# Kernel tuning notes

Measured on AMD Instinct MI355X. Metric: run time of the kernel, lower is better.

Reference implementation:

```python
import jax, jax.numpy as jnp
from jax import lax
import numpy as np

# Model dims (see shape_source)
D_MODEL = 768
N_LAYERS = 8
D_STATE = 16
EXPAND = 2
D_INNER = EXPAND * D_MODEL          # 1536
DT_RANK = (D_MODEL + 15) // 16       # 48
D_CONV = 4
PATCH = 16
IMG = 224
CH = 3
BATCH = 8


def rmsnorm(x, w, eps=1e-5):
    return x * lax.rsqrt(jnp.mean(x * x, axis=-1, keepdims=True) + eps) * w


def patch_embed(img, w, b):
    # img: [B,C,H,W] -> tokens [B, N, d_model]
    x = lax.conv_general_dilated(img, w, (PATCH, PATCH), 'VALID',
                                 dimension_numbers=('NCHW', 'OIHW', 'NCHW'))
    x = x + b[None, :, None, None]
    Bsz = img.shape[0]
    return x.reshape(Bsz, D_MODEL, -1).transpose(0, 2, 1)


def mamba_block(x, in_w, cw, cb, xw, dtw, dtb, a_log, d_p, ow):
    # x: [B, L, d_model]
    Bsz, L, _ = x.shape
    xz = x @ in_w.T                                   # [B,L,2*ED]
    xin, z = jnp.split(xz, 2, axis=-1)
    # causal depthwise conv over L
    xc = lax.conv_general_dilated(xin.transpose(0, 2, 1), cw, (1,),
                                  [(D_CONV - 1, 0)],
                                  dimension_numbers=('NCH', 'OIH', 'NCH'),
                                  feature_group_count=D_INNER)
    xin = jax.nn.silu((xc + cb[None, :, None]).transpose(0, 2, 1))  # [B,L,ED]
    dbc = xin @ xw.T                                  # [B,L,dt_rank+2N]
    delta, Bm, Cm = jnp.split(dbc, [DT_RANK, DT_RANK + D_STATE], axis=-1)
    delta = jax.nn.softplus(delta @ dtw.T + dtb)      # [B,L,ED]
    A = -jnp.exp(a_log)                               # [ED,N]
    dA = jnp.exp(delta[..., None] * A)                # [B,L,ED,N]
    dBx = (delta * xin)[..., None] * Bm[:, :, None, :]  # [B,L,ED,N]

    def step(h, inp):
        a, bx = inp
        h = a * h + bx
        return h, h

    h0 = jnp.zeros((Bsz, D_INNER, D_STATE), x.dtype)
    _, hs = lax.scan(step, h0, (dA.transpose(1, 0, 2, 3), dBx.transpose(1, 0, 2, 3)))
    y = jnp.einsum('lben,bln->ble', hs, Cm)           # [B,L,ED]
    y = y + d_p * xin
    y = y * jax.nn.silu(z)
    return y @ ow.T                                   # [B,L,d_model]


def setup_inputs() -> dict:
    key = jax.random.key(0)
    ks = jax.random.split(key, 16)
    s = 0.02
    nl = N_LAYERS
    inp = {
        'rgb': jax.random.normal(ks[0], (BATCH, CH, IMG, IMG), jnp.float32),
        't': jax.random.normal(ks[1], (BATCH, CH, IMG, IMG), jnp.float32),
        'pe_w': jax.random.normal(ks[2], (D_MODEL, CH, PATCH, PATCH), jnp.float32) * s,
        'pe_b': jnp.zeros((D_MODEL,), jnp.float32),
        'in_proj_w': jax.random.normal(ks[3], (nl, 2 * D_INNER, D_MODEL), jnp.float32) * s,
        'conv_w': jax.random.normal(ks[4], (nl, D_INNER, 1, D_CONV), jnp.float32) * s,
        'conv_b': jnp.zeros((nl, D_INNER), jnp.float32),
        'x_proj_w': jax.random.normal(ks[5], (nl, DT_RANK + 2 * D_STATE, D_INNER), jnp.float32) * s,
        'dt_proj_w': jax.random.normal(ks[6], (nl, D_INNER, DT_RANK), jnp.float32) * s,
        'dt_proj_b': jax.random.normal(ks[7], (nl, D_INNER), jnp.float32) * s,
        'A_log': jnp.log(jnp.broadcast_to(jnp.arange(1.0, D_STATE + 1.0), (nl, D_INNER, D_STATE))),
        'D': jnp.ones((nl, D_INNER), jnp.float32),
        'out_proj_w': jax.random.normal(ks[8], (nl, D_MODEL, D_INNER), jnp.float32) * s,
        'norm_w': jnp.ones((nl, D_MODEL), jnp.float32),
    }
    return inp


def reference(rgb, t, pe_w, pe_b, in_proj_w, conv_w, conv_b, x_proj_w,
              dt_proj_w, dt_proj_b, A_log, D, out_proj_w, norm_w):
    rt = patch_embed(rgb, pe_w, pe_b)   # [B,196,768]
    tt = patch_embed(t, pe_w, pe_b)
    x = jnp.concatenate([rt, tt], axis=1)  # [B,392,768]
    for i in range(N_LAYERS):
        x = x + mamba_block(rmsnorm(x, norm_w[i]), in_proj_w[i], conv_w[i],
                            conv_b[i], x_proj_w[i], dt_proj_w[i], dt_proj_b[i],
                            A_log[i], D[i], out_proj_w[i])
    Bsz = rgb.shape[0]
    # [B,2N,D] -> [B,2N,D,1] -> transpose(0,3) -> [1,2N,D,B] -> [2B,C,H,W]
    out = jnp.transpose(x[..., None], (3, 1, 2, 0)).reshape(2 * Bsz, CH, IMG, IMG)
    return out[:Bsz], out[Bsz:]
```

## Files before the change

kernel.cpp:

```cpp
#include <hip/hip_runtime.h>
#include <cstddef>
#include <cstdint>

#define L_TOK 392
#define BATCH 8
#define DM    768
#define ED    1536
#define NST   16
#define DTR   48
#define ROWS  (BATCH * L_TOK)

#define C_CH 8
#define CLEN 49
#define EGB  24

#define XP_Z  6


typedef unsigned short ushortT;
typedef __bf16 bf16x8 __attribute__((ext_vector_type(8)));
typedef unsigned short us8 __attribute__((ext_vector_type(8)));
typedef unsigned short us4 __attribute__((ext_vector_type(4)));
typedef float f32x4 __attribute__((ext_vector_type(4)));

#define LOG2E 1.4426950408889634f

__device__ __forceinline__ float bf2f(ushortT u) {
    union { unsigned int i; float f; } v; v.i = ((unsigned int)u) << 16; return v.f;
}
__device__ __forceinline__ ushortT f2bf(float f) {
    union { float f; unsigned int i; } v; v.f = f;
    unsigned int r = v.i + 0x7FFFu + ((v.i >> 16) & 1u);
    return (ushortT)(r >> 16);
}

__device__ __forceinline__ void gload16(const void* g, void* l) {
    __builtin_amdgcn_global_load_lds(
        (const __attribute__((address_space(1))) void*)g,
        (__attribute__((address_space(3))) void*)l, 16, 0, 0);
}

enum { EPI_STORE = 0, EPI_BIAS = 1, EPI_BIAS_SOFTPLUS = 2, EPI_ADD = 3 };

__global__ __launch_bounds__(256)
void convert3_kernel(const float* __restrict__ s0, ushortT* __restrict__ d0, int n0,
                     const float* __restrict__ s1, ushortT* __restrict__ d1, int n1,
                     const float* __restrict__ s2, ushortT* __restrict__ d2, int n2)
{
    int idx = blockIdx.x * 256 + threadIdx.x;
    const float* s; ushortT* d;
    if (idx < n0) { s = s0; d = d0; }
    else if (idx < n0 + n1) { idx -= n0; s = s1; d = d1; }
    else if (idx < n0 + n1 + n2) { idx -= n0 + n1; s = s2; d = d2; }
    else return;
    float4 f = *(const float4*)(s + (size_t)idx * 4);
    us4 h; h.x = f2bf(f.x); h.y = f2bf(f.y); h.z = f2bf(f.z); h.w = f2bf(f.w);
    *(us4*)(d + (size_t)idx * 4) = h;
}

template <int EPI, bool C_BF, bool SPLIT, bool ATOMIC, bool PARTIAL>
__global__ __launch_bounds__(256)
void gemm_mfma(const ushortT* __restrict__ A, int lda,
               const ushortT* __restrict__ W, int ldw,
               const float* __restrict__ bias,
               void* __restrict__ Cv, void* __restrict__ Cv2, int ldc,
               int M, int N, int K, int kchunk)
{
    __shared__ ushortT As[2][128 * 32];
    __shared__ ushortT Ws[2][128 * 32];

    const int tid  = threadIdx.x;
    const int lane = tid & 63;
    const int wave = tid >> 6;
    const int wm   = wave >> 1;
    const int wn   = wave & 1;
    const int quad = lane >> 4;
    const int l16  = lane & 15;

    const int gx   = gridDim.x;
    const int nwg  = gx * gridDim.y;
    const int flat = blockIdx.y * gx + blockIdx.x;
    const int q = nwg >> 3, r = nwg & 7;
    const int xcd = flat & 7, sidx = flat >> 3;
    const int swz = (xcd < r ? xcd * (q + 1) : r * (q + 1) + (xcd - r) * q) + sidx;

    const int m0 = (swz / gx) * 128;
    const int n0 = (swz % gx) * 128;
    const int kb = blockIdx.z * kchunk;
    const int KT = kchunk / 32;

    const int srow = lane >> 2;
    const int scol = (lane & 3) * 8;
    const ushortT* aBase = A + (size_t)(m0 + srow) * lda + scol;
    const ushortT* wBase = W + (size_t)(n0 + srow) * ldw + scol;

    auto stage = [&](int buf, int k0) {
#pragma unroll
        for (int c = 0; c < 2; ++c) {
            const int seg = wave * 2 + c;
            gload16(aBase + (size_t)(seg * 16) * lda + k0, &As[buf][seg * 512]);
            gload16(wBase + (size_t)(seg * 16) * ldw + k0, &Ws[buf][seg * 512]);
        }
    };

    f32x4 acc[4][4] = {};

    auto compute = [&](int buf) {
        bf16x8 af[4], bw[4];
#pragma unroll
        for (int t = 0; t < 4; ++t) {
            us8 ta = *(const us8*)&As[buf][(wm * 64 + t * 16 + l16) * 32 + quad * 8];
            af[t] = __builtin_bit_cast(bf16x8, ta);
            us8 tb = *(const us8*)&Ws[buf][(wn * 64 + t * 16 + l16) * 32 + quad * 8];
            bw[t] = __builtin_bit_cast(bf16x8, tb);
        }
#pragma unroll
        for (int i = 0; i < 4; ++i)
#pragma unroll
            for (int j = 0; j < 4; ++j)
                acc[i][j] = __builtin_amdgcn_mfma_f32_16x16x32_bf16(
                    af[i], bw[j], acc[i][j], 0, 0, 0);
    };

    stage(0, kb);
    __syncthreads();

    for (int kt = 0; kt < KT; ++kt) {
        if (kt + 1 < KT) stage((kt & 1) ^ 1, kb + (kt + 1) * 32);
        compute(kt & 1);
        __syncthreads();
    }

#pragma unroll
    for (int i = 0; i < 4; ++i) {
#pragma unroll
        for (int r2 = 0; r2 < 4; ++r2) {
            int gm = m0 + wm * 64 + i * 16 + quad * 4 + r2;
            if (gm >= M) continue;
#pragma unroll
            for (int j = 0; j < 4; ++j) {
                int gn = n0 + wn * 64 + j * 16 + l16;
                if (gn >= N) continue;
                float v = acc[i][j][r2];
                if (EPI == EPI_BIAS) v += bias[gn];
                void* dst = Cv;
                int cn = gn;
                if (SPLIT && gn >= ED) { dst = Cv2; cn = gn - ED; }
                size_t off = (size_t)gm * ldc + cn;
                if (PARTIAL) {
                    ((float*)dst)[(size_t)blockIdx.z * M * ldc + off] = v;
                } else if (ATOMIC) {
                    atomicAdd((float*)dst + off, v);
                } else if (C_BF) {
                    ((ushortT*)dst)[off] = f2bf(v);
                } else {
                    float* p = (float*)dst + off;
                    *p = (EPI == EPI_ADD) ? v + *p : v;
                }
            }
        }
    }
}

__global__ __launch_bounds__(256)
void reduce_partials_kernel(const float* __restrict__ P, float* __restrict__ dbc)
{
    int idx = blockIdx.x * 256 + threadIdx.x;
    if (idx >= ROWS * 80) return;
    float s = 0.f;
#pragma unroll
    for (int z = 0; z < XP_Z; ++z)
        s += P[(size_t)z * ROWS * 80 + idx];
    dbc[idx] = s;
}

template <int EPI, bool A_BF, bool C_BF>
__global__ __launch_bounds__(256)
void gemm_nt(const void* __restrict__ Av, int lda,
             const float* __restrict__ W, int ldw,
             const float* __restrict__ bias,
             void* __restrict__ Cv, int ldc,
             int M, int N, int K)
{
    __shared__ float As[16][68];
    __shared__ float Bs[16][68];
    const int tid = threadIdx.x;
    const int tx  = tid & 15;
    const int ty  = tid >> 4;
    const int bm  = blockIdx.y * 64;
    const int bn  = blockIdx.x * 64;
    const int lr  = tid >> 2;
    const int lk  = (tid & 3) * 4;

    float acc[4][4] = {};

    for (int k0 = 0; k0 < K; k0 += 16) {
        float a0 = 0.f, a1 = 0.f, a2 = 0.f, a3 = 0.f;
        float w0 = 0.f, w1 = 0.f, w2 = 0.f, w3 = 0.f;
        int ga = bm + lr;
        if (ga < M) {
            if (A_BF) {
                const ushortT* A = (const ushortT*)Av;
                ushort4 t = *(const ushort4*)(A + (size_t)ga * lda + k0 + lk);
                a0 = bf2f(t.x); a1 = bf2f(t.y); a2 = bf2f(t.z); a3 = bf2f(t.w);
            } else {
                const float* A = (const float*)Av;
                float4 t = *(const float4*)(A + (size_t)ga * lda + k0 + lk);
                a0 = t.x; a1 = t.y; a2 = t.z; a3 = t.w;
            }
        }
        int gw = bn + lr;
        if (gw < N) {
            float4 t = *(const float4*)(W + (size_t)gw * ldw + k0 + lk);
            w0 = t.x; w1 = t.y; w2 = t.z; w3 = t.w;
        }
        As[lk + 0][lr] = a0; As[lk + 1][lr] = a1;
        As[lk + 2][lr] = a2; As[lk + 3][lr] = a3;
        Bs[lk + 0][lr] = w0; Bs[lk + 1][lr] = w1;
        Bs[lk + 2][lr] = w2; Bs[lk + 3][lr] = w3;
        __syncthreads();
#pragma unroll
        for (int k = 0; k < 16; ++k) {
            float4 a4 = *(const float4*)&As[k][ty * 4];
            float4 b4 = *(const float4*)&Bs[k][tx * 4];
            float a[4] = {a4.x, a4.y, a4.z, a4.w};
            float b[4] = {b4.x, b4.y, b4.z, b4.w};
#pragma unroll
            for (int i = 0; i < 4; ++i)
#pragma unroll
                for (int j = 0; j < 4; ++j)
                    acc[i][j] += a[i] * b[j];
        }
        __syncthreads();
    }

#pragma unroll
    for (int i = 0; i < 4; ++i) {
        int gm = bm + ty * 4 + i;
        if (gm >= M) continue;
#pragma unroll
        for (int j = 0; j < 4; ++j) {
            int gn = bn + tx * 4 + j;
            if (gn >= N) continue;
            float v = acc[i][j];
            if (EPI == EPI_BIAS) v += bias[gn];
            if (EPI == EPI_BIAS_SOFTPLUS) {
                v += bias[gn];
                v = fmaxf(v, 0.f) + log1pf(expf(-fabsf(v)));
            }
            size_t off = (size_t)gm * ldc + gn;
            if (C_BF) {
                ((ushortT*)Cv)[off] = f2bf(v);
            } else {
                float* p = (float*)Cv + off;
                *p = (EPI == EPI_ADD) ? v + *p : v;
            }
        }
    }
}

__global__ __launch_bounds__(256)
void rmsnorm_kernel(const float* __restrict__ x, const float* __restrict__ w,
                    ushortT* __restrict__ xn)
{
    int r = blockIdx.x;
    const float* xr = x + (size_t)r * DM;
    float v[3];
    float s = 0.f;
#pragma unroll
    for (int i = 0; i < 3; ++i) {
        v[i] = xr[threadIdx.x + i * 256];
        s += v[i] * v[i];
    }
#pragma unroll
    for (int o = 32; o > 0; o >>= 1) s += __shfl_down(s, o, 64);
    __shared__ float wsum[4];
    __shared__ float scale_s;
    int wave = threadIdx.x >> 6;
    if ((threadIdx.x & 63) == 0) wsum[wave] = s;
    __syncthreads();
    if (threadIdx.x == 0) {
        float t = wsum[0] + wsum[1] + wsum[2] + wsum[3];
        scale_s = rsqrtf(t * (1.f / 768.f) + 1e-5f);
    }
    __syncthreads();
    float sc = scale_s;
#pragma unroll
    for (int i = 0; i < 3; ++i) {
        int d = threadIdx.x + i * 256;
        xn[(size_t)r * DM + d] = f2bf(v[i] * sc * w[d]);
    }
}

__global__ __launch_bounds__(256)
void conv_silu_kernel(const ushortT* __restrict__ xc, const float* __restrict__ cw,
                      const float* __restrict__ cb, ushortT* __restrict__ xin)
{
    int idx = blockIdx.x * 256 + threadIdx.x;
    if (idx >= ROWS * ED) return;
    int e = idx % ED;
    int r = idx / ED;
    int l = r % L_TOK;
    float w0 = cw[e * 4 + 0], w1 = cw[e * 4 + 1];
    float w2 = cw[e * 4 + 2], w3 = cw[e * 4 + 3];
    const ushortT* base = xc + (size_t)r * ED + e;
    float acc = cb[e] + w3 * bf2f(base[0]);
    if (l >= 1) acc += w2 * bf2f(base[-(ptrdiff_t)ED]);
    if (l >= 2) acc += w1 * bf2f(base[-(ptrdiff_t)(2 * ED)]);
    if (l >= 3) acc += w0 * bf2f(base[-(ptrdiff_t)(3 * ED)]);
    xin[(size_t)r * ED + e] = f2bf(acc / (1.f + __expf(-acc)));
}

__global__ __launch_bounds__(64)
void scan_part1(const ushortT* __restrict__ delta, const ushortT* __restrict__ xin,
                const float* __restrict__ dbc, const float* __restrict__ a_log,
                float* __restrict__ hend, float* __restrict__ sdl)
{
    __shared__ float BsL[CLEN * 16];
    const int tid = threadIdx.x;
    const int bid = blockIdx.x;
    const int eg = bid % EGB;
    const int c  = (bid / EGB) % C_CH;
    const int b  = bid / (EGB * C_CH);
    const int e  = eg * 64 + tid;
    const int l0 = c * CLEN;
    const int rb = b * L_TOK + l0;

    for (int i = tid; i < CLEN * 16; i += 64) {
        int s = i >> 4, n = i & 15;
        BsL[i] = dbc[(size_t)(rb + s) * 80 + 48 + n];
    }
    __syncthreads();

    float a[16];
    const float* ar = a_log + (size_t)e * 16;
#pragma unroll
    for (int n = 0; n < 16; ++n) a[n] = -__expf(ar[n]) * LOG2E;

    float h[16];
#pragma unroll
    for (int n = 0; n < 16; ++n) h[n] = 0.f;
    float sum_dl = 0.f;

    const size_t base = (size_t)rb * ED + e;
    float rdl[7], rxi[7];
#pragma unroll
    for (int j = 0; j < 7; ++j) {
        rdl[j] = bf2f(delta[base + (size_t)j * ED]);
        rxi[j] = bf2f(xin[base + (size_t)j * ED]);
    }
    for (int s0 = 0; s0 < CLEN; s0 += 7) {
#pragma unroll
        for (int j = 0; j < 7; ++j) {
            const int s = s0 + j;
            float dl = rdl[j], xi = rxi[j];
            int sp = s + 7; if (sp > CLEN - 1) sp = CLEN - 1;
            rdl[j] = bf2f(delta[base + (size_t)sp * ED]);
            rxi[j] = bf2f(xin[base + (size_t)sp * ED]);
            float dlxi = dl * xi;
            sum_dl += dl;
#pragma unroll
            for (int n = 0; n < 16; ++n)
                h[n] = __builtin_amdgcn_exp2f(dl * a[n]) * h[n] + dlxi * BsL[s * 16 + n];
        }
    }

    float* hp = hend + (((size_t)b * ED + e) * C_CH + c) * 16;
#pragma unroll
    for (int n = 0; n < 16; ++n) hp[n] = h[n];
    sdl[((size_t)b * ED + e) * C_CH + c] = sum_dl;
}

__global__ __launch_bounds__(64)
void scan_part2(const ushortT* __restrict__ delta, const ushortT* __restrict__ xin,
                const float* __restrict__ dbc, const ushortT* __restrict__ zb,
                const float* __restrict__ a_log, const float* __restrict__ dvec,
                const float* __restrict__ hend, const float* __restrict__ sdl,
                ushortT* __restrict__ y)
{
    __shared__ float BsL[CLEN * 16];
    __shared__ float CsL[CLEN * 16];
    const int tid = threadIdx.x;
    const int bid = blockIdx.x;
    const int eg = bid % EGB;
    const int c  = (bid / EGB) % C_CH;
    const int b  = bid / (EGB * C_CH);
    const int e  = eg * 64 + tid;
    const int l0 = c * CLEN;
    const int rb = b * L_TOK + l0;

    for (int i = tid; i < CLEN * 16; i += 64) {
        int s = i >> 4, n = i & 15;
        size_t row = (size_t)(rb + s) * 80;
        BsL[i] = dbc[row + 48 + n];
        CsL[i] = dbc[row + 64 + n];
    }
    __syncthreads();

    float a[16];
    const float* ar = a_log + (size_t)e * 16;
#pragma unroll
    for (int n = 0; n < 16; ++n) a[n] = -__expf(ar[n]) * LOG2E;
    const float dcf = dvec[e];

    float h[16];
#pragma unroll
    for (int n = 0; n < 16; ++n) h[n] = 0.f;
    const float* hb = hend + (((size_t)b * ED + e) * C_CH) * 16;
    const float* sb = sdl + ((size_t)b * ED + e) * C_CH;
    for (int cc = 0; cc < c; ++cc) {
        float sv = sb[cc];
#pragma unroll
        for (int n = 0; n < 16; ++n)
            h[n] = __builtin_amdgcn_exp2f(a[n] * sv) * h[n] + hb[cc * 16 + n];
    }

    const size_t base = (size_t)rb * ED + e;
    float rdl[7], rxi[7], rz[7];
#pragma unroll
    for (int j = 0; j < 7; ++j) {
        rdl[j] = bf2f(delta[base + (size_t)j * ED]);
        rxi[j] = bf2f(xin[base + (size_t)j * ED]);
        rz[j]  = bf2f(zb[base + (size_t)j * ED]);
    }
    for (int s0 = 0; s0 < CLEN; s0 += 7) {
#pragma unroll
        for (int j = 0; j < 7; ++j) {
            const int s = s0 + j;
            float dl = rdl[j], xi = rxi[j], z = rz[j];
            int sp = s + 7; if (sp > CLEN - 1) sp = CLEN - 1;
            rdl[j] = bf2f(delta[base + (size_t)sp * ED]);
            rxi[j] = bf2f(xin[base + (size_t)sp * ED]);
            rz[j]  = bf2f(zb[base + (size_t)sp * ED]);
            float dlxi = dl * xi;
            float yv = 0.f;
#pragma unroll
            for (int n = 0; n < 16; ++n) {
                h[n] = __builtin_amdgcn_exp2f(dl * a[n]) * h[n] + dlxi * BsL[s * 16 + n];
                yv += h[n] * CsL[s * 16 + n];
            }
            yv += dcf * xi;
            float sz = z / (1.f + __expf(-z));
            y[base + (size_t)s * ED] = f2bf(yv * sz);
        }
    }
}

__global__ __launch_bounds__(256)
void im2col_kernel(const float* __restrict__ rgb, const float* __restrict__ timg,
                   ushortT* __restrict__ P)
{
    int idx = blockIdx.x * 256 + threadIdx.x;
    if (idx >= ROWS * DM) return;
    int k = idx % DM;
    int r = idx / DM;
    int b = r / L_TOK;
    int l = r % L_TOK;
    const float* img = (l < 196) ? rgb : timg;
    int p  = (l < 196) ? l : l - 196;
    int py = p / 14, px = p % 14;
    int c  = k >> 8;
    int ph = (k >> 4) & 15;
    int pw = k & 15;
    P[idx] = f2bf(img[(((size_t)b * 3 + c) * 224 + (py * 16 + ph)) * 224 + (px * 16 + pw)]);
}

__global__ __launch_bounds__(256)
void out_transpose_kernel(const float* __restrict__ x, float* __restrict__ out)
{
    int idx = blockIdx.x * 256 + threadIdx.x;
    if (idx >= ROWS * DM) return;
    int b = idx & 7;
    int d = (idx >> 3) % DM;
    int l = idx / (8 * DM);
    out[idx] = x[((size_t)(b * L_TOK + l)) * DM + d];
}

extern "C" void kernel_launch(void* const* d_in, const int* in_sizes, int n_in,
                              void* d_out, int out_size, void* d_ws, size_t ws_size,
                              hipStream_t stream)
{
    (void)in_sizes; (void)n_in; (void)out_size; (void)ws_size;

    const float* rgb  = (const float*)d_in[0];
    const float* timg = (const float*)d_in[1];
    const float* pe_w = (const float*)d_in[2];
    const float* pe_b = (const float*)d_in[3];
    const float* in_w = (const float*)d_in[4];
    const float* cw   = (const float*)d_in[5];
    const float* cb   = (const float*)d_in[6];
    const float* xw   = (const float*)d_in[7];
    const float* dtw  = (const float*)d_in[8];
    const float* dtb  = (const float*)d_in[9];
    const float* alog = (const float*)d_in[10];
    const float* dvec = (const float*)d_in[11];
    const float* ow   = (const float*)d_in[12];
    const float* nw   = (const float*)d_in[13];

    char* p = (char*)d_ws;
    float*   X   = (float*)p;    p += (size_t)ROWS * DM * 4;
    ushortT* XC  = (ushortT*)p;  p += (size_t)ROWS * ED * 2;
    ushortT* Zb  = (ushortT*)p;  p += (size_t)ROWS * ED * 2;
    ushortT* XIN = (ushortT*)p;  p += (size_t)ROWS * ED * 2;
    ushortT* DEL = (ushortT*)p;  p += (size_t)ROWS * ED * 2;
    float*   DBC = (float*)p;    p += (size_t)ROWS * 80 * 4;
    ushortT* XN  = DEL;

    ushortT* INWB = XIN;
    ushortT* XWB  = (ushortT*)DBC;
    ushortT* PEB  = Zb;

    float* POUT = (float*)d_out;
    float* HEND = (float*)d_out;
    float* SDL  = HEND + (size_t)BATCH * ED * C_CH * 16;
    ushortT* OWB = (ushortT*)((char*)d_out +
                   ((size_t)BATCH * ED * C_CH * 16 + (size_t)BATCH * ED * C_CH) * 4);

    dim3 b256(256);
    const int MT = (ROWS + 127) / 128;
    const int SCAN_BLOCKS = BATCH * C_CH * EGB;

    const int PE_F4  = DM * DM / 4;
    const int INW_F4 = 2 * ED * DM / 4;
    const int XW_F4  = 80 * ED / 4;
    const int OW_F4  = DM * ED / 4;
    const int CVT_BLOCKS = (INW_F4 + XW_F4 + OW_F4 + 255) / 256;

    convert3_kernel<<<(PE_F4 + 255) / 256, b256, 0, stream>>>(
        pe_w, PEB, PE_F4, nullptr, nullptr, 0, nullptr, nullptr, 0);
    im2col_kernel<<<(ROWS * DM + 255) / 256, b256, 0, stream>>>(rgb, timg, XC);
    gemm_mfma<EPI_BIAS, false, false, false, false><<<dim3(DM / 128, MT), b256, 0, stream>>>(
        XC, DM, PEB, DM, pe_b, X, nullptr, DM, ROWS, DM, DM, DM);

    for (int i = 0; i < 8; ++i) {
        const float* in_wi = in_w + (size_t)i * 2 * ED * DM;
        const float* cwi   = cw   + (size_t)i * ED * 4;
        const float* cbi   = cb   + (size_t)i * ED;
        const float* xwi   = xw   + (size_t)i * 80 * ED;
        const float* dtwi  = dtw  + (size_t)i * ED * DTR;
        const float* dtbi  = dtb  + (size_t)i * ED;
        const float* ali   = alog + (size_t)i * ED * NST;
        const float* dvi   = dvec + (size_t)i * ED;
        const float* owi   = ow   + (size_t)i * DM * ED;
        const float* nwi   = nw   + (size_t)i * DM;

        convert3_kernel<<<CVT_BLOCKS, b256, 0, stream>>>(
            in_wi, INWB, INW_F4, xwi, XWB, XW_F4, owi, OWB, OW_F4);
        rmsnorm_kernel<<<ROWS, b256, 0, stream>>>(X, nwi, XN);
        gemm_mfma<EPI_STORE, true, true, false, false><<<dim3(2 * ED / 128, MT), b256, 0, stream>>>(
            XN, DM, INWB, DM, nullptr, XC, Zb, ED, ROWS, 2 * ED, DM, DM);
        conv_silu_kernel<<<(ROWS * ED + 255) / 256, b256, 0, stream>>>(
            XC, cwi, cbi, XIN);
        gemm_mfma<EPI_STORE, false, false, false, true><<<dim3(1, MT, XP_Z), b256, 0, stream>>>(
            XIN, ED, XWB, ED, nullptr, POUT, nullptr, 80, ROWS, 80, ED, ED / XP_Z);
        reduce_partials_kernel<<<(ROWS * 80 + 255) / 256, b256, 0, stream>>>(
            POUT, DBC);
        gemm_nt<EPI_BIAS_SOFTPLUS, false, true><<<dim3(ED / 64, ROWS / 64), b256, 0, stream>>>(
            DBC, 80, dtwi, DTR, dtbi, DEL, ED, ROWS, ED, DTR);
        scan_part1<<<SCAN_BLOCKS, 64, 0, stream>>>(
            DEL, XIN, DBC, ali, HEND, SDL);
        scan_part2<<<SCAN_BLOCKS, 64, 0, stream>>>(
            DEL, XIN, DBC, Zb, ali, dvi, HEND, SDL, XC);
        gemm_mfma<EPI_ADD, false, false, true, false><<<dim3(DM / 128, MT, 2), b256, 0, stream>>>(
            XC, ED, OWB, ED, nullptr, X, nullptr, DM, ROWS, DM, ED, ED / 2);
    }

    out_transpose_kernel<<<(ROWS * DM + 255) / 256, b256, 0, stream>>>(
        X, (float*)d_out);
}
```

Before: 1.733 ms.

## Move dt_proj GEMM to bf16 MFMA and fuse rmsnorm with weight conversion

Replaces the scalar fp32 gemm_nt used for dt_proj (K=48) with the MFMA bf16 GEMM. The reduce kernel now also writes a bf16 copy of the delta rank slice padded to 64 columns, and the dt_proj weights are converted to a zero-padded bf16 layout. Softplus is added to the MFMA epilogue. Rmsnorm and the per-layer weight conversion are merged into one prep kernel to cut a launch per layer. The cost is a bf16 rounding of the delta inputs and weights, plus extra buffers placed in the output scratch space.

Result: slower. 1.793 ms (+3.4%).

```diff
diff --git a/kernel.cpp b/kernel.cpp
--- a/kernel.cpp
+++ b/kernel.cpp
@@ -58,6 +58,71 @@
     *(us4*)(d + (size_t)idx * 4) = h;
 }
 
+#define INW_F4 (2 * ED * DM / 4)
+#define XW_F4  (80 * ED / 4)
+#define OW_F4  (DM * ED / 4)
+#define DTW_U  (ED * 16)
+
+__global__ __launch_bounds__(256)
+void prep_kernel(const float* __restrict__ in_w, ushortT* __restrict__ inwb,
+                 const float* __restrict__ xw,   ushortT* __restrict__ xwb,
+                 const float* __restrict__ ow,   ushortT* __restrict__ owb,
+                 const float* __restrict__ dtw,  ushortT* __restrict__ dtwb,
+                 const float* __restrict__ x,    const float* __restrict__ nw,
+                 ushortT* __restrict__ xn)
+{
+    if (blockIdx.x < ROWS) {
+        int r = blockIdx.x;
+        const float* xr = x + (size_t)r * DM;
+        float v[3];
+        float s = 0.f;
+#pragma unroll
+        for (int i = 0; i < 3; ++i) {
+            v[i] = xr[threadIdx.x + i * 256];
+            s += v[i] * v[i];
+        }
+#pragma unroll
+        for (int o = 32; o > 0; o >>= 1) s += __shfl_down(s, o, 64);
+        __shared__ float wsum[4];
+        __shared__ float scale_s;
+        int wave = threadIdx.x >> 6;
+        if ((threadIdx.x & 63) == 0) wsum[wave] = s;
+        __syncthreads();
+        if (threadIdx.x == 0) {
+            float t = wsum[0] + wsum[1] + wsum[2] + wsum[3];
+            scale_s = rsqrtf(t * (1.f / 768.f) + 1e-5f);
+        }
+        __syncthreads();
+        float sc = scale_s;
+#pragma unroll
+        for (int i = 0; i < 3; ++i) {
+            int d = threadIdx.x + i * 256;
+            xn[(size_t)r * DM + d] = f2bf(v[i] * sc * nw[d]);
+        }
+        return;
+    }
+    int idx = (blockIdx.x - ROWS) * 256 + threadIdx.x;
+    if (idx < INW_F4 + XW_F4 + OW_F4) {
+        const float* s; ushortT* d;
+        if (idx < INW_F4) { s = in_w; d = inwb; }
+        else if (idx < INW_F4 + XW_F4) { idx -= INW_F4; s = xw; d = xwb; }
+        else { idx -= INW_F4 + XW_F4; s = ow; d = owb; }
+        float4 f = *(const float4*)(s + (size_t)idx * 4);
+        us4 h; h.x = f2bf(f.x); h.y = f2bf(f.y); h.z = f2bf(f.z); h.w = f2bf(f.w);
+        *(us4*)(d + (size_t)idx * 4) = h;
+    } else if (idx < INW_F4 + XW_F4 + OW_F4 + DTW_U) {
+        int u = idx - (INW_F4 + XW_F4 + OW_F4);
+        int row = u >> 4;
+        int c4  = (u & 15) * 4;
+        us4 h = {0, 0, 0, 0};
+        if (c4 < DTR) {
+            float4 f = *(const float4*)(dtw + (size_t)row * DTR + c4);
+            h.x = f2bf(f.x); h.y = f2bf(f.y); h.z = f2bf(f.z); h.w = f2bf(f.w);
+        }
+        *(us4*)(dtwb + (size_t)row * 64 + c4) = h;
+    }
+}
+
 template <int EPI, bool C_BF, bool SPLIT, bool ATOMIC, bool PARTIAL>
 __global__ __launch_bounds__(256)
 void gemm_mfma(const ushortT* __restrict__ A, int lda,
@@ -143,6 +208,10 @@
                 if (gn >= N) continue;
                 float v = acc[i][j][r2];
                 if (EPI == EPI_BIAS) v += bias[gn];
+                if (EPI == EPI_BIAS_SOFTPLUS) {
+                    v += bias[gn];
+                    v = fmaxf(v, 0.f) + log1pf(expf(-fabsf(v)));
+                }
                 void* dst = Cv;
                 int cn = gn;
                 if (SPLIT && gn >= ED) { dst = Cv2; cn = gn - ED; }
@@ -163,132 +232,24 @@
 }
 
 __global__ __launch_bounds__(256)
-void reduce_partials_kernel(const float* __restrict__ P, float* __restrict__ dbc)
+void reduce_partials_kernel(const float* __restrict__ P, float* __restrict__ dbc,
+                            ushortT* __restrict__ dbc48)
 {
     int idx = blockIdx.x * 256 + threadIdx.x;
-    if (idx >= ROWS * 80) return;
-    float s = 0.f;
-#pragma unroll
-    for (int z = 0; z < XP_Z; ++z)
-        s += P[(size_t)z * ROWS * 80 + idx];
-    dbc[idx] = s;
-}
-
-template <int EPI, bool A_BF, bool C_BF>
-__global__ __launch_bounds__(256)
-void gemm_nt(const void* __restrict__ Av, int lda,
-             const float* __restrict__ W, int ldw,
-             const float* __restrict__ bias,
-             void* __restrict__ Cv, int ldc,
-             int M, int N, int K)
-{
-    __shared__ float As[16][68];
-    __shared__ float Bs[16][68];
-    const int tid = threadIdx.x;
-    const int tx  = tid & 15;
-    const int ty  = tid >> 4;
-    const int bm  = blockIdx.y * 64;
-    const int bn  = blockIdx.x * 64;
-    const int lr  = tid >> 2;
-    const int lk  = (tid & 3) * 4;
-
-    float acc[4][4] = {};
-
-    for (int k0 = 0; k0 < K; k0 += 16) {
-        float a0 = 0.f, a1 = 0.f, a2 = 0.f, a3 = 0.f;
-        float w0 = 0.f, w1 = 0.f, w2 = 0.f, w3 = 0.f;
-        int ga = bm + lr;
-        if (ga < M) {
-            if (A_BF) {
-                const ushortT* A = (const ushortT*)Av;
-                ushort4 t = *(const ushort4*)(A + (size_t)ga * lda + k0 + lk);
-                a0 = bf2f(t.x); a1 = bf2f(t.y); a2 = bf2f(t.z); a3 = bf2f(t.w);
-            } else {
-                const float* A = (const float*)Av;
-                float4 t = *(const float4*)(A + (size_t)ga * lda + k0 + lk);
-                a0 = t.x; a1 = t.y; a2 = t.z; a3 = t.w;
-            }
-        }
-        int gw = bn + lr;
-        if (gw < N) {
-            float4 t = *(const float4*)(W + (size_t)gw * ldw + k0 + lk);
-            w0 = t.x; w1 = t.y; w2 = t.z; w3 = t.w;
-        }
-        As[lk + 0][lr] = a0; As[lk + 1][lr] = a1;
-        As[lk + 2][lr] = a2; As[lk + 3][lr] = a3;
-        Bs[lk + 0][lr] = w0; Bs[lk + 1][lr] = w1;
-        Bs[lk + 2][lr] = w2; Bs[lk + 3][lr] = w3;
-        __syncthreads();
-#pragma unroll
-        for (int k = 0; k < 16; ++k) {
-            float4 a4 = *(const float4*)&As[k][ty * 4];
-            float4 b4 = *(const float4*)&Bs[k][tx * 4];
-            float a[4] = {a4.x, a4.y, a4.z, a4.w};
-            float b[4] = {b4.x, b4.y, b4.z, b4.w};
-#pragma unroll
-            for (int i = 0; i < 4; ++i)
-#pragma unroll
-                for (int j = 0; j < 4; ++j)
-                    acc[i][j] += a[i] * b[j];
-        }
-        __syncthreads();
-    }
-
-#pragma unroll
-    for (int i = 0; i < 4; ++i) {
-        int gm = bm + ty * 4 + i;
-        if (gm >= M) continue;
-#pragma unroll
-        for (int j = 0; j < 4; ++j) {
-            int gn = bn + tx * 4 + j;
-            if (gn >= N) continue;
-            float v = acc[i][j];
-            if (EPI == EPI_BIAS) v += bias[gn];
-            if (EPI == EPI_BIAS_SOFTPLUS) {
-                v += bias[gn];
-                v = fmaxf(v, 0.f) + log1pf(expf(-fabsf(v)));
-            }
-            size_t off = (size_t)gm * ldc + gn;
-            if (C_BF) {
-                ((ushortT*)Cv)[off] = f2bf(v);
-            } else {
-                float* p = (float*)Cv + off;
-                *p = (EPI == EPI_ADD) ? v + *p : v;
-            }
-        }
-    }
-}
-
-__global__ __launch_bounds__(256)
-void rmsnorm_kernel(const float* __restrict__ x, const float* __restrict__ w,
-                    ushortT* __restrict__ xn)
-{
-    int r = blockIdx.x;
-    const float* xr = x + (size_t)r * DM;
-    float v[3];
-    float s = 0.f;
-#pragma unroll
-    for (int i = 0; i < 3; ++i) {
-        v[i] = xr[threadIdx.x + i * 256];
-        s += v[i] * v[i];
-    }
-#pragma unroll
-    for (int o = 32; o > 0; o >>= 1) s += __shfl_down(s, o, 64);
-    __shared__ float wsum[4];
-    __shared__ float scale_s;
-    int wave = threadIdx.x >> 6;
-    if ((threadIdx.x & 63) == 0) wsum[wave] = s;
-    __syncthreads();
-    if (threadIdx.x == 0) {
-        float t = wsum[0] + wsum[1] + wsum[2] + wsum[3];
-        scale_s = rsqrtf(t * (1.f / 768.f) + 1e-5f);
-    }
-    __syncthreads();
-    float sc = scale_s;
-#pragma unroll
-    for (int i = 0; i < 3; ++i) {
-        int d = threadIdx.x + i * 256;
-        xn[(size_t)r * DM + d] = f2bf(v[i] * sc * w[d]);
+    if (idx < ROWS * 80) {
+        float s = 0.f;
+#pragma unroll
+        for (int z = 0; z < XP_Z; ++z)
+            s += P[(size_t)z * ROWS * 80 + idx];
+        dbc[idx] = s;
+        int r = idx / 80, c = idx % 80;
+        if (c < DTR) dbc48[(size_t)r * 64 + c] = f2bf(s);
+    } else {
+        int t = idx - ROWS * 80;
+        if (t < ROWS * 16) {
+            int r = t >> 4, c = DTR + (t & 15);
+            dbc48[(size_t)r * 64 + c] = 0;
+        }
     }
 }
 
@@ -513,18 +474,17 @@
     float* POUT = (float*)d_out;
     float* HEND = (float*)d_out;
     float* SDL  = HEND + (size_t)BATCH * ED * C_CH * 16;
+    ushortT* DBC48 = (ushortT*)((char*)d_out + (size_t)XP_Z * ROWS * 80 * 4);
+    ushortT* DTWB  = DBC48 + (size_t)ROWS * 64;
     ushortT* OWB = (ushortT*)((char*)d_out +
                    ((size_t)BATCH * ED * C_CH * 16 + (size_t)BATCH * ED * C_CH) * 4);
 
     dim3 b256(256);
     const int MT = (ROWS + 127) / 128;
     const int SCAN_BLOCKS = BATCH * C_CH * EGB;
-
-    const int PE_F4  = DM * DM / 4;
-    const int INW_F4 = 2 * ED * DM / 4;
-    const int XW_F4  = 80 * ED / 4;
-    const int OW_F4  = DM * ED / 4;
-    const int CVT_BLOCKS = (INW_F4 + XW_F4 + OW_F4 + 255) / 256;
+    const int PE_F4 = DM * DM / 4;
+    const int PREP_BLOCKS = ROWS + (INW_F4 + XW_F4 + OW_F4 + DTW_U + 255) / 256;
+    const int RED_BLOCKS = (ROWS * 96 + 255) / 256;
 
     convert3_kernel<<<(PE_F4 + 255) / 256, b256, 0, stream>>>(
         pe_w, PEB, PE_F4, nullptr, nullptr, 0, nullptr, nullptr, 0);
@@ -544,19 +504,18 @@
         const float* owi   = ow   + (size_t)i * DM * ED;
         const float* nwi   = nw   + (size_t)i * DM;
 
-        convert3_kernel<<<CVT_BLOCKS, b256, 0, stream>>>(
-            in_wi, INWB, INW_F4, xwi, XWB, XW_F4, owi, OWB, OW_F4);
-        rmsnorm_kernel<<<ROWS, b256, 0, stream>>>(X, nwi, XN);
+        prep_kernel<<<PREP_BLOCKS, b256, 0, stream>>>(
+            in_wi, INWB, xwi, XWB, owi, OWB, dtwi, DTWB, X, nwi, XN);
         gemm_mfma<EPI_STORE, true, true, false, false><<<dim3(2 * ED / 128, MT), b256, 0, stream>>>(
             XN, DM, INWB, DM, nullptr, XC, Zb, ED, ROWS, 2 * ED, DM, DM);
         conv_silu_kernel<<<(ROWS * ED + 255) / 256, b256, 0, stream>>>(
             XC, cwi, cbi, XIN);
         gemm_mfma<EPI_STORE, false, false, false, true><<<dim3(1, MT, XP_Z), b256, 0, stream>>>(
             XIN, ED, XWB, ED, nullptr, POUT, nullptr, 80, ROWS, 80, ED, ED / XP_Z);
-        reduce_partials_kernel<<<(ROWS * 80 + 255) / 256, b256, 0, stream>>>(
-            POUT, DBC);
-        gemm_nt<EPI_BIAS_SOFTPLUS, false, true><<<dim3(ED / 64, ROWS / 64), b256, 0, stream>>>(
-            DBC, 80, dtwi, DTR, dtbi, DEL, ED, ROWS, ED, DTR);
+        reduce_partials_kernel<<<RED_BLOCKS, b256, 0, stream>>>(
+            POUT, DBC, DBC48);
+        gemm_mfma<EPI_BIAS_SOFTPLUS, true, false, false, false><<<dim3(ED / 128, MT), b256, 0, stream>>>(
+            DBC48, 64, DTWB, 64, dtbi, DEL, nullptr, ED, ROWS, ED, 64, 64);
         scan_part1<<<SCAN_BLOCKS, 64, 0, stream>>>(
             DEL, XIN, DBC, ali, HEND, SDL);
         scan_part2<<<SCAN_BLOCKS, 64, 0, stream>>>(
```
